# Optimization experiments

Measured on AMD Instinct MI355X. Metric: run time of the kernel, lower is better.

The kernel has to match this reference:

```python
import jax, jax.numpy as jnp
import numpy as np
from jax import lax

B, C, N = 8, 3, 65536
NUM_POINTS = 1024


def setup_inputs() -> dict:
    key = jax.random.key(0)
    points = jax.random.normal(key, (B, C, N), dtype=jnp.float32)
    return {"points": points}


def furthest_point_sampling(xyz, num_points):
    # xyz: (B, N, 3) -> indices (B, num_points), int32
    b, n, _ = xyz.shape
    init_idx = jnp.zeros((b,), dtype=jnp.int32)  # CUDA FPS seeds with index 0
    init_dists = jnp.full((b, n), 1e10, dtype=xyz.dtype)

    def step(carry, _):
        dists, last_idx = carry
        last_pt = jnp.take_along_axis(xyz, last_idx[:, None, None], axis=1)  # (B,1,3)
        d = jnp.sum(jnp.square(xyz - last_pt), axis=-1)  # (B,N) squared dist to newest pt
        dists = jnp.minimum(dists, d)
        nxt = jnp.argmax(dists, axis=-1).astype(jnp.int32)
        return (dists, nxt), nxt

    (_, _), rest = lax.scan(step, (init_dists, init_idx), None, length=num_points - 1)
    # rest: (num_points-1, B) -> (B, num_points)
    idx = jnp.concatenate([init_idx[None, :], rest], axis=0).T
    return idx


def reference(points):
    # points: (B, 3, N), channels-first as in the torch module
    xyz = jnp.transpose(points, (0, 2, 1))  # (B, N, 3)
    idx = furthest_point_sampling(xyz, NUM_POINTS)  # (B, num_points)
    # fps_gather_by_index: gather along point axis of (B, 3, N)
    new_points = jnp.take_along_axis(points, idx[:, None, :], axis=2)  # (B, 3, num_points)
    return new_points
```

## Files before the change

kernel.cpp:

```cpp
#include <hip/hip_runtime.h>


namespace {

constexpr int kB = 8;
constexpr int kN = 65536;
constexpr int kNP = 1024;
constexpr int kPB = 16;
constexpr int kThreads = 256;
constexpr int kPPT = kN / (kPB * kThreads);
constexpr int kGrp = kPPT / 4;
constexpr int kWaves = kThreads / 64;
constexpr int kRgn = 16;
constexpr int kRgnStride = 32;
constexpr int kBlocks = 256;

template <int CTRL>
__device__ __forceinline__ unsigned long long dpp_max_u64(unsigned long long k) {
  const int lo = (int)(unsigned)k;
  const int hi = (int)(unsigned)(k >> 32);
  const unsigned plo = (unsigned)__builtin_amdgcn_update_dpp(lo, lo, CTRL, 0xF, 0xF, false);
  const unsigned phi = (unsigned)__builtin_amdgcn_update_dpp(hi, hi, CTRL, 0xF, 0xF, false);
  const unsigned long long p = ((unsigned long long)phi << 32) | plo;
  return p > k ? p : k;
}

__device__ __forceinline__ unsigned long long load_l2(const unsigned long long* p) {
  unsigned long long v;
  asm volatile("global_load_dwordx2 %0, %1, off sc0\n\ts_waitcnt vmcnt(0)"
               : "=v"(v)
               : "v"(p)
               : "memory");
  return v;
}

__device__ __forceinline__ void store_l2(unsigned long long* p, unsigned long long v) {
  asm volatile("global_store_dwordx2 %0, %1, off sc0" ::"v"(p), "v"(v) : "memory");
}

__global__ __launch_bounds__(kThreads) void fps_kernel(const float* __restrict__ pts,
                                                       float* __restrict__ out,
                                                       unsigned long long* __restrict__ slots,
                                                       unsigned* __restrict__ ctrl) {
  const int tid = threadIdx.x;
  const int lane = tid & 63;
  const int wave = tid >> 6;

  __shared__ int s_batch, s_slice;
  __shared__ unsigned long long s_wkey[kWaves];
  __shared__ unsigned s_win[2];
  __shared__ float s_qc[2][3];
  __shared__ int s_hist[kNP];

  if (tid == 0) {
    unsigned xcc;
    asm volatile("s_getreg_b32 %0, hwreg(HW_REG_XCC_ID)" : "=s"(xcc));
    const int home = (int)(xcc & 7u);
    int batch = -1, slice = -1;
    const int pos = (int)atomicAdd(&ctrl[home], 1u);
    if (pos < kPB) {
      batch = home;
      slice = pos;
    }
    __hip_atomic_fetch_add(&ctrl[8], 1u, __ATOMIC_RELEASE, __HIP_MEMORY_SCOPE_AGENT);
    if (batch < 0) {
      while (__hip_atomic_load(&ctrl[8], __ATOMIC_ACQUIRE, __HIP_MEMORY_SCOPE_AGENT) <
             (unsigned)kBlocks) {
        __builtin_amdgcn_s_sleep(8);
      }
      int need = (int)atomicAdd(&ctrl[9], 1u);
      for (int j = 0; j < kB; ++j) {
        int have = (int)__hip_atomic_load(&ctrl[j], __ATOMIC_RELAXED, __HIP_MEMORY_SCOPE_AGENT);
        have = have > kPB ? kPB : have;
        const int vac = kPB - have;
        if (need < vac) {
          batch = j;
          slice = have + need;
          break;
        }
        need -= vac;
      }
    }
    s_batch = batch;
    s_slice = slice;
    s_win[0] = 0xFFFFFFFFu;
    s_win[1] = 0xFFFFFFFFu;
  }
  __syncthreads();

  const int batch = s_batch;
  const int slice = s_slice;
  if (batch < 0) return;

  const float* __restrict__ xb = pts + (size_t)batch * 3 * kN;
  const float* __restrict__ yb = xb + kN;
  const float* __restrict__ zb = xb + 2 * kN;

  const int sbase = slice * (kThreads * kPPT);
  const int base0 = sbase + tid * 4;
  float px[kPPT], py[kPPT], pz[kPPT], dist[kPPT];
#pragma unroll
  for (int g = 0; g < kGrp; ++g) {
    const int base = base0 + g * (kThreads * 4);
    const float4 vx = *reinterpret_cast<const float4*>(xb + base);
    const float4 vy = *reinterpret_cast<const float4*>(yb + base);
    const float4 vz = *reinterpret_cast<const float4*>(zb + base);
    px[g * 4 + 0] = vx.x; px[g * 4 + 1] = vx.y; px[g * 4 + 2] = vx.z; px[g * 4 + 3] = vx.w;
    py[g * 4 + 0] = vy.x; py[g * 4 + 1] = vy.y; py[g * 4 + 2] = vy.z; py[g * 4 + 3] = vy.w;
    pz[g * 4 + 0] = vz.x; pz[g * 4 + 1] = vz.y; pz[g * 4 + 2] = vz.z; pz[g * 4 + 3] = vz.w;
  }
#pragma unroll
  for (int k = 0; k < kPPT; ++k) dist[k] = 1e10f;

  float qx = xb[0], qy = yb[0], qz = zb[0];

  unsigned long long* const sb = slots + (size_t)batch * kRgn * kRgnStride;

  for (int it = 1; it < kNP; ++it) {
    float bd = -1.0f;
    int bi = 0;
#pragma unroll
    for (int g = 0; g < kGrp; ++g) {
#pragma unroll
      for (int j = 0; j < 4; ++j) {
        const int k = g * 4 + j;
        const float dx = px[k] - qx;
        const float dy = py[k] - qy;
        const float dz = pz[k] - qz;
        const float ss =
            __fadd_rn(__fadd_rn(__fmul_rn(dx, dx), __fmul_rn(dy, dy)), __fmul_rn(dz, dz));
        const float nd = fminf(dist[k], ss);
        dist[k] = nd;
        if (nd > bd) {
          bd = nd;
          bi = base0 + g * (kThreads * 4) + j;
        }
      }
    }

    unsigned long long key = ((unsigned long long)__float_as_uint(bd) << 32) |
                             ((unsigned long long)(0xFFFFu - (unsigned)bi) << 16) |
                             (unsigned long long)(unsigned)it;

    key = dpp_max_u64<0x111>(key);
    key = dpp_max_u64<0x112>(key);
    key = dpp_max_u64<0x114>(key);
    key = dpp_max_u64<0x118>(key);
    key = dpp_max_u64<0x142>(key);
    key = dpp_max_u64<0x143>(key);
    const unsigned wklo = (unsigned)__builtin_amdgcn_readlane((int)(unsigned)key, 63);
    const unsigned wkhi = (unsigned)__builtin_amdgcn_readlane((int)(unsigned)(key >> 32), 63);
    if (lane == 0) {
      s_wkey[wave] = ((unsigned long long)wkhi << 32) | wklo;
    }
    __syncthreads();

    if (wave == 0) {
      unsigned long long bk = s_wkey[lane & (kWaves - 1)];
      bk = dpp_max_u64<0xB1>(bk);
      bk = dpp_max_u64<0x4E>(bk);

      unsigned long long* const rgn = sb + (size_t)(it & (kRgn - 1)) * kRgnStride;
      if (lane == 0) {
        store_l2(rgn + slice, bk);
        __hip_atomic_store(rgn + kPB + slice, bk, __ATOMIC_RELAXED,
                           __HIP_MEMORY_SCOPE_AGENT);
      }

      unsigned long long sv;
      int round = 0;
      for (;;) {
        unsigned long long a = load_l2(rgn + (lane & (kPB - 1)));
        bool ok = (unsigned)(a & 0xFFFFull) == (unsigned)it;
        if (round >= 2 && !ok) {
          const unsigned long long fb = __hip_atomic_load(
              rgn + kPB + (lane & (kPB - 1)), __ATOMIC_RELAXED, __HIP_MEMORY_SCOPE_AGENT);
          if ((unsigned)(fb & 0xFFFFull) == (unsigned)it) {
            a = fb;
            ok = true;
          }
        }
        if (__all(ok)) {
          sv = a;
          break;
        }
        ++round;
      }

      const int cand = (int)(0xFFFFu - ((unsigned)(sv >> 16) & 0xFFFFu));
      const float gx = xb[cand];
      const float gy = yb[cand];
      const float gz = zb[cand];

      unsigned long long k2 = sv;
      k2 = dpp_max_u64<0xB1>(k2);
      k2 = dpp_max_u64<0x4E>(k2);
      k2 = dpp_max_u64<0x141>(k2);
      k2 = dpp_max_u64<0x140>(k2);

      const unsigned long long m = __ballot(sv == k2);
      const int src = (int)__ffsll(m) - 1;
      qx = __int_as_float(__builtin_amdgcn_readlane(__float_as_int(gx), src));
      qy = __int_as_float(__builtin_amdgcn_readlane(__float_as_int(gy), src));
      qz = __int_as_float(__builtin_amdgcn_readlane(__float_as_int(gz), src));

      const int wi = (int)(0xFFFFu - ((unsigned)(k2 >> 16) & 0xFFFFu));
      if (lane == 0) {
        s_hist[it] = wi;
        s_qc[it & 1][0] = qx;
        s_qc[it & 1][1] = qy;
        s_qc[it & 1][2] = qz;
        __hip_atomic_store(&s_win[it & 1], ((unsigned)wi << 16) | (unsigned)it,
                           __ATOMIC_RELEASE, __HIP_MEMORY_SCOPE_WORKGROUP);
      }
    } else {
      unsigned v;
      do {
        v = __hip_atomic_load(&s_win[it & 1], __ATOMIC_ACQUIRE, __HIP_MEMORY_SCOPE_WORKGROUP);
      } while ((v & 0xFFFFu) != (unsigned)it);
      qx = s_qc[it & 1][0];
      qy = s_qc[it & 1][1];
      qz = s_qc[it & 1][2];
    }
  }

  __syncthreads();

  if (slice == 0) {
    float* __restrict__ ob = out + (size_t)batch * 3 * kNP;
    for (int j = tid; j < kNP; j += kThreads) {
      const int id = (j == 0) ? 0 : s_hist[j];
      ob[j] = xb[id];
      ob[kNP + j] = yb[id];
      ob[2 * kNP + j] = zb[id];
    }
  }
}

}

extern "C" void kernel_launch(void* const* d_in, const int* in_sizes, int n_in,
                              void* d_out, int out_size, void* d_ws, size_t ws_size,
                              hipStream_t stream) {
  (void)in_sizes;
  (void)n_in;
  (void)out_size;
  (void)ws_size;
  const float* pts = (const float*)d_in[0];
  float* out = (float*)d_out;
  unsigned* ctrl = (unsigned*)d_ws;
  unsigned long long* slots = (unsigned long long*)((char*)d_ws + 1024);
  hipMemsetAsync(d_ws, 0, 64, stream);
  fps_kernel<<<dim3(kBlocks), dim3(kThreads), 0, stream>>>(pts, out, slots, ctrl);
}
```

Baseline: 1.489 ms.

## Publish per-wave keys to global slots and drop per-iteration block barrier

```diff
diff --git a/kernel.cpp b/kernel.cpp
--- a/kernel.cpp
+++ b/kernel.cpp
@@ -11,8 +11,10 @@
 constexpr int kPPT = kN / (kPB * kThreads);
 constexpr int kGrp = kPPT / 4;
 constexpr int kWaves = kThreads / 64;
-constexpr int kRgn = 16;
-constexpr int kRgnStride = 32;
+constexpr int kSlots = kPB * kWaves;
+constexpr int kRgn = 4;
+constexpr int kRgnStride = 2 * kSlots;
+constexpr int kBatchStride = kRgn * kRgnStride;
 constexpr int kBlocks = 256;
 
 template <int CTRL>
@@ -25,6 +27,17 @@
   return p > k ? p : k;
 }
 
+__device__ __forceinline__ unsigned long long readlane_u64(unsigned long long v, int l) {
+  const unsigned lo = (unsigned)__builtin_amdgcn_readlane((int)(unsigned)v, l);
+  const unsigned hi = (unsigned)__builtin_amdgcn_readlane((int)(unsigned)(v >> 32), l);
+  return ((unsigned long long)hi << 32) | lo;
+}
+
+__device__ __forceinline__ unsigned long long u64max(unsigned long long a,
+                                                     unsigned long long b) {
+  return a > b ? a : b;
+}
+
 __device__ __forceinline__ unsigned long long load_l2(const unsigned long long* p) {
   unsigned long long v;
   asm volatile("global_load_dwordx2 %0, %1, off sc0\n\ts_waitcnt vmcnt(0)"
@@ -47,9 +60,7 @@
   const int wave = tid >> 6;
 
   __shared__ int s_batch, s_slice;
-  __shared__ unsigned long long s_wkey[kWaves];
-  __shared__ unsigned s_win[2];
-  __shared__ float s_qc[2][3];
+  __shared__ unsigned long long s_mail[2][3];
   __shared__ int s_hist[kNP];
 
   if (tid == 0) {
@@ -83,8 +94,8 @@
     }
     s_batch = batch;
     s_slice = slice;
-    s_win[0] = 0xFFFFFFFFu;
-    s_win[1] = 0xFFFFFFFFu;
+    s_mail[0][0] = s_mail[0][1] = s_mail[0][2] = 0xFFFFFFFF00000000ull;
+    s_mail[1][0] = s_mail[1][1] = s_mail[1][2] = 0xFFFFFFFF00000000ull;
   }
   __syncthreads();
 
@@ -114,7 +125,8 @@
 
   float qx = xb[0], qy = yb[0], qz = zb[0];
 
-  unsigned long long* const sb = slots + (size_t)batch * kRgn * kRgnStride;
+  unsigned long long* const sb = slots + (size_t)batch * kBatchStride;
+  const int slot = slice * kWaves + wave;
 
   for (int it = 1; it < kNP; ++it) {
     float bd = -1.0f;
@@ -148,33 +160,24 @@
     key = dpp_max_u64<0x118>(key);
     key = dpp_max_u64<0x142>(key);
     key = dpp_max_u64<0x143>(key);
-    const unsigned wklo = (unsigned)__builtin_amdgcn_readlane((int)(unsigned)key, 63);
-    const unsigned wkhi = (unsigned)__builtin_amdgcn_readlane((int)(unsigned)(key >> 32), 63);
-    if (lane == 0) {
-      s_wkey[wave] = ((unsigned long long)wkhi << 32) | wklo;
-    }
-    __syncthreads();
+
+    unsigned long long* const rgn = sb + (size_t)(it & (kRgn - 1)) * kRgnStride;
+
+    if (lane == 63) {
+      store_l2(rgn + slot, key);
+      __hip_atomic_store(rgn + kSlots + slot, key, __ATOMIC_RELAXED,
+                         __HIP_MEMORY_SCOPE_AGENT);
+    }
 
     if (wave == 0) {
-      unsigned long long bk = s_wkey[lane & (kWaves - 1)];
-      bk = dpp_max_u64<0xB1>(bk);
-      bk = dpp_max_u64<0x4E>(bk);
-
-      unsigned long long* const rgn = sb + (size_t)(it & (kRgn - 1)) * kRgnStride;
-      if (lane == 0) {
-        store_l2(rgn + slice, bk);
-        __hip_atomic_store(rgn + kPB + slice, bk, __ATOMIC_RELAXED,
-                           __HIP_MEMORY_SCOPE_AGENT);
-      }
-
       unsigned long long sv;
       int round = 0;
       for (;;) {
-        unsigned long long a = load_l2(rgn + (lane & (kPB - 1)));
+        unsigned long long a = load_l2(rgn + lane);
         bool ok = (unsigned)(a & 0xFFFFull) == (unsigned)it;
         if (round >= 2 && !ok) {
           const unsigned long long fb = __hip_atomic_load(
-              rgn + kPB + (lane & (kPB - 1)), __ATOMIC_RELAXED, __HIP_MEMORY_SCOPE_AGENT);
+              rgn + kSlots + lane, __ATOMIC_RELAXED, __HIP_MEMORY_SCOPE_AGENT);
           if ((unsigned)(fb & 0xFFFFull) == (unsigned)it) {
             a = fb;
             ok = true;
@@ -197,30 +200,42 @@
       k2 = dpp_max_u64<0x4E>(k2);
       k2 = dpp_max_u64<0x141>(k2);
       k2 = dpp_max_u64<0x140>(k2);
-
-      const unsigned long long m = __ballot(sv == k2);
+      const unsigned long long r0 = readlane_u64(k2, 0);
+      const unsigned long long r1 = readlane_u64(k2, 16);
+      const unsigned long long r2 = readlane_u64(k2, 32);
+      const unsigned long long r3 = readlane_u64(k2, 48);
+      const unsigned long long win = u64max(u64max(r0, r1), u64max(r2, r3));
+
+      const unsigned long long m = __ballot(sv == win);
       const int src = (int)__ffsll(m) - 1;
       qx = __int_as_float(__builtin_amdgcn_readlane(__float_as_int(gx), src));
       qy = __int_as_float(__builtin_amdgcn_readlane(__float_as_int(gy), src));
       qz = __int_as_float(__builtin_amdgcn_readlane(__float_as_int(gz), src));
 
-      const int wi = (int)(0xFFFFu - ((unsigned)(k2 >> 16) & 0xFFFFu));
       if (lane == 0) {
-        s_hist[it] = wi;
-        s_qc[it & 1][0] = qx;
-        s_qc[it & 1][1] = qy;
-        s_qc[it & 1][2] = qz;
-        __hip_atomic_store(&s_win[it & 1], ((unsigned)wi << 16) | (unsigned)it,
-                           __ATOMIC_RELEASE, __HIP_MEMORY_SCOPE_WORKGROUP);
+        const int p = it & 1;
+        const unsigned long long t = (unsigned long long)(unsigned)it << 32;
+        __hip_atomic_store(&s_mail[p][0], t | (unsigned)__float_as_uint(qx),
+                           __ATOMIC_RELAXED, __HIP_MEMORY_SCOPE_WORKGROUP);
+        __hip_atomic_store(&s_mail[p][1], t | (unsigned)__float_as_uint(qy),
+                           __ATOMIC_RELAXED, __HIP_MEMORY_SCOPE_WORKGROUP);
+        __hip_atomic_store(&s_mail[p][2], t | (unsigned)__float_as_uint(qz),
+                           __ATOMIC_RELAXED, __HIP_MEMORY_SCOPE_WORKGROUP);
+        s_hist[it] = (int)(0xFFFFu - ((unsigned)(win >> 16) & 0xFFFFu));
       }
     } else {
-      unsigned v;
+      const int p = it & 1;
+      unsigned long long w0, w1, w2;
       do {
-        v = __hip_atomic_load(&s_win[it & 1], __ATOMIC_ACQUIRE, __HIP_MEMORY_SCOPE_WORKGROUP);
-      } while ((v & 0xFFFFu) != (unsigned)it);
-      qx = s_qc[it & 1][0];
-      qy = s_qc[it & 1][1];
-      qz = s_qc[it & 1][2];
+        w0 = __hip_atomic_load(&s_mail[p][0], __ATOMIC_RELAXED, __HIP_MEMORY_SCOPE_WORKGROUP);
+        w1 = __hip_atomic_load(&s_mail[p][1], __ATOMIC_RELAXED, __HIP_MEMORY_SCOPE_WORKGROUP);
+        w2 = __hip_atomic_load(&s_mail[p][2], __ATOMIC_RELAXED, __HIP_MEMORY_SCOPE_WORKGROUP);
+      } while (!((unsigned)(w0 >> 32) == (unsigned)it &&
+                 (unsigned)(w1 >> 32) == (unsigned)it &&
+                 (unsigned)(w2 >> 32) == (unsigned)it));
+      qx = __int_as_float((int)(unsigned)w0);
+      qy = __int_as_float((int)(unsigned)w1);
+      qz = __int_as_float((int)(unsigned)w2);
     }
   }
 
```

New measurement: 1.769 ms. +18.8%, slower.
